# Kernel optimization log

Measured on AMD Instinct MI355X. Metric: run time of the kernel, lower is better.

The kernel has to match this reference:

```python
import jax, jax.numpy as jnp
import numpy as np

EMBED_DIM = 96
OUT_DIM = 192
HEADS = 2
HEAD_DIM = OUT_DIM // HEADS  # 96
STRIDE_Q = (1, 2, 2)
STRIDE_KV = (1, 8, 8)
SCALE = 1.0 / float(np.sqrt(HEAD_DIM))


def layer_norm(x, g, b, eps=1e-5):
    m = jnp.mean(x, -1, keepdims=True)
    v = jnp.mean(jnp.square(x - m), -1, keepdims=True)
    return (x - m) * jax.lax.rsqrt(v + eps) * g + b


def pool(x, thw, conv_w, g, b, stride):
    # x: [B, heads, N, d] with cls token at position 0; depthwise conv3d pool + LayerNorm(d)
    B, nh, N, d = x.shape
    T, H, W = thw
    cls_tok, rest = x[:, :, :1], x[:, :, 1:]
    rest = rest.transpose(0, 1, 3, 2).reshape(B * nh, d, T, H, W)
    rest = jax.lax.conv_general_dilated(
        rest, conv_w, stride, [(1, 1), (1, 1), (1, 1)],
        dimension_numbers=('NCDHW', 'OIDHW', 'NCDHW'), feature_group_count=d)
    T2, H2, W2 = rest.shape[2], rest.shape[3], rest.shape[4]
    rest = rest.reshape(B, nh, d, -1).transpose(0, 1, 3, 2)
    x = jnp.concatenate([cls_tok, rest], axis=2)
    return layer_norm(x, g, b), (T2, H2, W2)


def rel_idx(q_n, k_n):
    # decomposed relative-distance indices with q/k resolution ratio scaling
    q_r = max(k_n / q_n, 1.0)
    k_r = max(q_n / k_n, 1.0)
    d = (jnp.arange(q_n, dtype=jnp.float32)[:, None] * q_r
         - jnp.arange(k_n, dtype=jnp.float32)[None, :] * k_r + (k_n - 1) * k_r)
    return d.astype(jnp.int32)


def add_rel_pos(attn, q, q_thw, k_thw, rph, rpw, rpt):
    qt, qh, qw = q_thw
    kt, kh, kw = k_thw
    Rh = rph[rel_idx(qh, kh)]  # [qh, kh, d]
    Rw = rpw[rel_idx(qw, kw)]  # [qw, kw, d]
    Rt = rpt[rel_idx(qt, kt)]  # [qt, kt, d]
    B, nh, qN, d = q.shape
    r_q = q[:, :, 1:].reshape(B, nh, qt, qh, qw, d)
    rel_h = jnp.einsum('bythwc,hkc->bythwk', r_q, Rh)  # k = kh
    rel_w = jnp.einsum('bythwc,wkc->bythwk', r_q, Rw)  # k = kw
    rel_t = jnp.einsum('bythwc,tkc->bythwk', r_q, Rt)  # k = kt
    rel = (rel_t[..., :, None, None] + rel_h[..., None, :, None]
           + rel_w[..., None, None, :]).reshape(B, nh, qt * qh * qw, kt * kh * kw)
    return attn.at[:, :, 1:, 1:].add(rel)


def _forward(x, qkv_w, qkv_b, proj_w, proj_b, pq_w, nq_g, nq_b, pk_w, nk_g, nk_b,
             pv_w, nv_g, nv_b, rel_pos_h, rel_pos_w, rel_pos_t, thw):
    B, N, C = x.shape
    qkv = (x @ qkv_w.T + qkv_b).reshape(B, N, 3, HEADS, HEAD_DIM).transpose(2, 0, 3, 1, 4)
    q, k, v = qkv[0], qkv[1], qkv[2]  # each [B, heads, N, head_dim]
    k, k_thw = pool(k, thw, pk_w, nk_g, nk_b, STRIDE_KV)
    v, _ = pool(v, thw, pv_w, nv_g, nv_b, STRIDE_KV)
    q, q_thw = pool(q, thw, pq_w, nq_g, nq_b, STRIDE_Q)
    attn = jnp.einsum('bhqd,bhkd->bhqk', q * SCALE, k)
    attn = add_rel_pos(attn, q, q_thw, k_thw, rel_pos_h, rel_pos_w, rel_pos_t)
    attn = jax.nn.softmax(attn, axis=-1)
    out = jnp.einsum('bhqk,bhkd->bhqd', attn, v) + q  # residual_pool, with cls embed
    out = out.transpose(0, 2, 1, 3).reshape(B, -1, OUT_DIM)
    return out @ proj_w.T + proj_b


def setup_inputs() -> dict:
    key = jax.random.key(0)
    ks = jax.random.split(key, 10)
    T, H, W = 8, 56, 56
    N = 1 + T * H * W  # 25089
    B = 4
    std = 0.02
    return {
        'x': jax.random.normal(ks[0], (B, N, EMBED_DIM), jnp.float32),
        'qkv_w': jax.random.normal(ks[1], (3 * OUT_DIM, EMBED_DIM), jnp.float32) * std,
        'qkv_b': jnp.zeros((3 * OUT_DIM,), jnp.float32),
        'proj_w': jax.random.normal(ks[2], (OUT_DIM, OUT_DIM), jnp.float32) * std,
        'proj_b': jnp.zeros((OUT_DIM,), jnp.float32),
        'pq_w': jax.random.normal(ks[3], (HEAD_DIM, 1, 3, 3, 3), jnp.float32) * std,
        'nq_g': jnp.ones((HEAD_DIM,), jnp.float32),
        'nq_b': jnp.zeros((HEAD_DIM,), jnp.float32),
        'pk_w': jax.random.normal(ks[4], (HEAD_DIM, 1, 3, 3, 3), jnp.float32) * std,
        'nk_g': jnp.ones((HEAD_DIM,), jnp.float32),
        'nk_b': jnp.zeros((HEAD_DIM,), jnp.float32),
        'pv_w': jax.random.normal(ks[5], (HEAD_DIM, 1, 3, 3, 3), jnp.float32) * std,
        'nv_g': jnp.ones((HEAD_DIM,), jnp.float32),
        'nv_b': jnp.zeros((HEAD_DIM,), jnp.float32),
        'rel_pos_h': jax.random.normal(ks[6], (55, HEAD_DIM), jnp.float32) * std,
        'rel_pos_w': jax.random.normal(ks[7], (55, HEAD_DIM), jnp.float32) * std,
        'rel_pos_t': jax.random.normal(ks[8], (15, HEAD_DIM), jnp.float32) * std,
        'thw_t': 8, 'thw_h': 56, 'thw_w': 56,
    }


def reference(x, qkv_w, qkv_b, proj_w, proj_b, pq_w, nq_g, nq_b, pk_w, nk_g, nk_b,
              pv_w, nv_g, nv_b, rel_pos_h, rel_pos_w, rel_pos_t, thw_t, thw_h, thw_w):
    thw = (int(thw_t), int(thw_h), int(thw_w))
    return _forward(x, qkv_w, qkv_b, proj_w, proj_b, pq_w, nq_g, nq_b, pk_w, nk_g, nk_b,
                    pv_w, nv_g, nv_b, rel_pos_h, rel_pos_w, rel_pos_t, thw)
```

## Files before the change

kernel.cpp:

```cpp
#include <hip/hip_runtime.h>
#include <hip/hip_bf16.h>

typedef short short8 __attribute__((ext_vector_type(8)));
typedef float floatx4 __attribute__((ext_vector_type(4)));
typedef float floatx4v __attribute__((ext_vector_type(4)));

#define SCALE_F 0.10206207261596575f
#define TOKSTRIDE 401424

static __device__ __forceinline__ float b2f(unsigned short u){
  unsigned int v = ((unsigned int)u) << 16; float f;
  __builtin_memcpy(&f, &v, 4); return f;
}
static __device__ __forceinline__ unsigned short f2b(float f){
  __hip_bfloat16 h = __float2bfloat16(f);
  unsigned short u; __builtin_memcpy(&u, &h, 2); return u;
}
static __device__ __forceinline__ int map20(int i){
  return (i < 2) ? i : 7 + ((i-2)/3)*8 + ((i-2)%3);
}

struct ConvDesc {
  const void* src[17];
  long long off[17];
  int count[17];
};

__global__ __launch_bounds__(256) void k_convert(ConvDesc d, unsigned short* dst_base,
                                                 int* flagp, const unsigned int* xprobe)
{
  __shared__ int sflag;
  if (threadIdx.x < 64){
    unsigned int w = xprobe[1024 + threadIdx.x];
    int e = (w >> 7) & 0xFF;
    int pl = (e >= 90 && e <= 140) ? 1 : 0;
    unsigned long long m = __ballot(pl);
    if (threadIdx.x == 0){
      sflag = (__popcll(m) < 40) ? 1 : 0;
      if (blockIdx.x == 0 && blockIdx.y == 0) *flagp = sflag;
    }
  }
  __syncthreads();
  const int flag = sflag;
  const int t = blockIdx.y + 1;
  const int cnt = d.count[t];
  unsigned short* dst = dst_base + d.off[t];
  const float* sf = (const float*)d.src[t];
  const unsigned short* su = (const unsigned short*)d.src[t];
  for (int i = blockIdx.x*blockDim.x + threadIdx.x; i < cnt; i += gridDim.x*blockDim.x){
    dst[i] = flag ? f2b(sf[i]) : su[i];
  }
}

static __device__ __forceinline__ void load_x_frag(
    const void* xr_, int flag, size_t elem_off, short8& a0, short8& a1, short8& a2)
{
  if (flag){
    const float* xr = (const float*)xr_ + elem_off;
    floatx4v f0 = *(const floatx4v*)(xr),      f1 = *(const floatx4v*)(xr+4);
    floatx4v f2 = *(const floatx4v*)(xr+32),   f3 = *(const floatx4v*)(xr+36);
    floatx4v f4 = *(const floatx4v*)(xr+64),   f5 = *(const floatx4v*)(xr+68);
    #pragma unroll
    for (int j = 0; j < 4; ++j){
      a0[j] = (short)f2b(f0[j]); a0[j+4] = (short)f2b(f1[j]);
      a1[j] = (short)f2b(f2[j]); a1[j+4] = (short)f2b(f3[j]);
      a2[j] = (short)f2b(f4[j]); a2[j+4] = (short)f2b(f5[j]);
    }
  } else {
    const unsigned short* xr = (const unsigned short*)xr_ + elem_off;
    a0 = *(const short8*)(xr);
    a1 = *(const short8*)(xr + 32);
    a2 = *(const short8*)(xr + 64);
  }
}

__global__ __launch_bounds__(256) void k_qkv(
    const void* __restrict__ x, const unsigned short* __restrict__ w,
    const unsigned short* __restrict__ bias, unsigned short* __restrict__ qr,
    unsigned short* __restrict__ kc, unsigned short* __restrict__ vc,
    unsigned short* __restrict__ kcls, unsigned short* __restrict__ vcls,
    const int* __restrict__ flagp)
{
  const int flag = *flagp;
  const int lane = threadIdx.x & 63;
  const int wv = threadIdx.x >> 6;
  const int kq = (lane >> 4) * 8;
  const int quad = lane >> 4;
  const int col_l = lane & 15;

  if (blockIdx.x < 1569){
    const int m_base = blockIdx.x * 64 + wv * 16;
    int ma = m_base + col_l; if (ma > 100355) ma = 100355;
    short8 a0, a1, a2;
    load_x_frag(x, flag, (size_t)ma*96 + kq, a0, a1, a2);

    int bbase[4], ntok[4], mrow[4];
    #pragma unroll
    for (int r = 0; r < 4; ++r){
      int m = m_base + quad*4 + r;
      mrow[r] = m;
      int bb = m / 25089;
      ntok[r] = m - bb*25089;
      bbase[r] = bb*2;
    }

    #pragma unroll
    for (int ct = 0; ct < 12; ++ct){
      int col = ct*16 + col_l;
      const unsigned short* wrow = w + col*96 + kq;
      short8 b0 = *(const short8*)(wrow);
      short8 b1 = *(const short8*)(wrow + 32);
      short8 b2 = *(const short8*)(wrow + 64);
      float bv = b2f(bias[col]);
      floatx4 acc = {0.f,0.f,0.f,0.f};
      acc = __builtin_amdgcn_mfma_f32_16x16x32_bf16(a0, b0, acc, 0,0,0);
      acc = __builtin_amdgcn_mfma_f32_16x16x32_bf16(a1, b1, acc, 0,0,0);
      acc = __builtin_amdgcn_mfma_f32_16x16x32_bf16(a2, b2, acc, 0,0,0);
      const int head = ct / 6;
      const int dt6  = ct % 6;
      #pragma unroll
      for (int r = 0; r < 4; ++r){
        if (mrow[r] < 100356)
          qr[(size_t)((bbase[r]+head)*6 + dt6)*TOKSTRIDE + (size_t)ntok[r]*16 + col_l]
            = f2b(acc[r] + bv);
      }
    }
  } else {
    const int id = blockIdx.x - 1569;
    const int isv = id / 201;
    const int bx = id - isv*201;
    const int rbase = bx * 64 + wv * 16;

    int rhoA = rbase + col_l; if (rhoA > 12803) rhoA = 12803;
    int bA, nA;
    if (rhoA < 4){ bA = rhoA; nA = 0; }
    else {
      int rp = rhoA - 4;
      bA = rp / 3200; int rem = rp - bA*3200;
      int t = rem / 400; int s = rem - t*400;
      int ry = s / 20, rx = s - ry*20;
      nA = 1 + (t*56 + map20(ry))*56 + map20(rx);
    }
    short8 a0, a1, a2;
    load_x_frag(x, flag, ((size_t)bA*25089 + nA)*96 + kq, a0, a1, a2);

    int isCls[4], bI[4], baseI[4], valid[4];
    #pragma unroll
    for (int r = 0; r < 4; ++r){
      int rho = rbase + quad*4 + r;
      valid[r] = (rho < 12804);
      if (rho > 12803) rho = 12803;
      if (rho < 4){ isCls[r] = 1; bI[r] = rho; baseI[r] = 0; }
      else {
        int rp = rho - 4;
        int b = rp / 3200; int rem = rp - b*3200;
        int t = rem / 400; int s = rem - t*400;
        int ry = s / 20, rx = s - ry*20;
        isCls[r] = 0; bI[r] = b;
        baseI[r] = (((b*8 + t)*20 + ry)*20 + rx)*192;
      }
    }

    unsigned short* buf  = isv ? vc : kc;
    unsigned short* bufc = isv ? vcls : kcls;
    #pragma unroll
    for (int ct = 0; ct < 12; ++ct){
      const int col = 192 + (isv*12 + ct)*16 + col_l;
      const unsigned short* wrow = w + col*96 + kq;
      short8 b0 = *(const short8*)(wrow);
      short8 b1 = *(const short8*)(wrow + 32);
      short8 b2 = *(const short8*)(wrow + 64);
      float bv = b2f(bias[col]);
      floatx4 acc = {0.f,0.f,0.f,0.f};
      acc = __builtin_amdgcn_mfma_f32_16x16x32_bf16(a0, b0, acc, 0,0,0);
      acc = __builtin_amdgcn_mfma_f32_16x16x32_bf16(a1, b1, acc, 0,0,0);
      acc = __builtin_amdgcn_mfma_f32_16x16x32_bf16(a2, b2, acc, 0,0,0);
      const int head = ct / 6;
      const int dstat = (ct % 6) * 16;
      #pragma unroll
      for (int r = 0; r < 4; ++r){
        if (valid[r]){
          float o = acc[r] + bv;
          if (isCls[r]) bufc[(bI[r]*2 + head)*96 + dstat + col_l] = f2b(o);
          else          buf[baseI[r] + head*96 + dstat + col_l]   = f2b(o);
        }
      }
    }
  }
}

__global__ __launch_bounds__(384) void k_pool(
    const unsigned short* __restrict__ qr, const unsigned short* __restrict__ cwq,
    const unsigned short* __restrict__ gq, const unsigned short* __restrict__ btaq,
    unsigned short* __restrict__ qp,
    const unsigned short* __restrict__ kc, const unsigned short* __restrict__ vc,
    const unsigned short* __restrict__ kcls, const unsigned short* __restrict__ vcls,
    const unsigned short* __restrict__ cwk, const unsigned short* __restrict__ gk, const unsigned short* __restrict__ bk,
    const unsigned short* __restrict__ cwv, const unsigned short* __restrict__ gv, const unsigned short* __restrict__ bv,
    unsigned short* __restrict__ kp, unsigned short* __restrict__ vt)
{
  const int tid = threadIdx.x;
  if (blockIdx.x < 1792){
    __shared__ float wlds[27*96];
    __shared__ float gls[96], bls[96];
    __shared__ float ls1[29*12], ls2[29*12];
    __shared__ float lmean[29], linvs[29];

    const int bid = blockIdx.x;
    const int y  = bid % 28;
    const int t  = (bid / 28) % 8;
    const int bh = bid / 224;
    const bool has_cls = (y == 0 && t == 0);

    for (int idx = tid; idx < 27*96; idx += 384){
      int tap = idx / 96, d = idx - tap*96;
      wlds[idx] = b2f(cwq[d*27 + tap]);
    }
    for (int idx = tid; idx < 96; idx += 384){
      gls[idx] = b2f(gq[idx]); bls[idx] = b2f(btaq[idx]);
    }
    __syncthreads();

    const int x = tid / 12, dg = tid - x*12;
    const unsigned short* rowb = qr + (size_t)(bh*6 + (dg >> 1))*TOKSTRIDE + (dg & 1)*8;
    float val[8] = {0,0,0,0,0,0,0,0};

    if (x < 28){
      #pragma unroll
      for (int dt = 0; dt < 3; ++dt){
        int tt = t + dt - 1; if (tt < 0 || tt >= 8) continue;
        #pragma unroll
        for (int dy = 0; dy < 3; ++dy){
          int yy = 2*y + dy - 1; if (yy < 0 || yy >= 56) continue;
          #pragma unroll
          for (int dx = 0; dx < 3; ++dx){
            int xv = 2*x + dx - 1; if (xv < 0 || xv >= 56) continue;
            const int tap = (dt*3+dy)*3+dx;
            short8 v = *(const short8*)(rowb + (size_t)(1 + (tt*56 + yy)*56 + xv)*16);
            const float* wr = wlds + tap*96 + dg*8;
            #pragma unroll
            for (int j = 0; j < 8; ++j) val[j] += b2f((unsigned short)v[j]) * wr[j];
          }
        }
      }
      float s1 = 0.f, s2 = 0.f;
      #pragma unroll
      for (int j = 0; j < 8; ++j){ s1 += val[j]; s2 += val[j]*val[j]; }
      ls1[x*12+dg] = s1; ls2[x*12+dg] = s2;
    } else if (has_cls && tid >= 348 && tid < 360){
      int cdg = tid - 348;
      const unsigned short* rowc = qr + (size_t)(bh*6 + (cdg >> 1))*TOKSTRIDE + (cdg & 1)*8;
      short8 v = *(const short8*)(rowc);
      float s1 = 0.f, s2 = 0.f;
      #pragma unroll
      for (int j = 0; j < 8; ++j){ val[j] = b2f((unsigned short)v[j]); s1 += val[j]; s2 += val[j]*val[j]; }
      ls1[28*12+cdg] = s1; ls2[28*12+cdg] = s2;
    }
    __syncthreads();

    if (tid < 28 || (tid == 28 && has_cls)){
      float s1 = 0.f, s2 = 0.f;
      #pragma unroll
      for (int k = 0; k < 12; ++k){ s1 += ls1[tid*12+k]; s2 += ls2[tid*12+k]; }
      float mean = s1 * (1.f/96.f);
      float var  = s2 * (1.f/96.f) - mean*mean;
      lmean[tid] = mean; linvs[tid] = rsqrtf(var + 1e-5f);
    }
    __syncthreads();

    if (x < 28){
      float mean = lmean[x], inv = linvs[x];
      int tok = 1 + (t*28 + y)*28 + x;
      short8 o;
      #pragma unroll
      for (int j = 0; j < 8; ++j)
        o[j] = (short)f2b((val[j] - mean)*inv*gls[dg*8+j] + bls[dg*8+j]);
      *(short8*)(qp + ((size_t)bh*6273 + tok)*96 + dg*8) = o;
    } else if (has_cls && tid >= 348 && tid < 360){
      int cdg = tid - 348;
      float mean = lmean[28], inv = linvs[28];
      short8 o;
      #pragma unroll
      for (int j = 0; j < 8; ++j)
        o[j] = (short)f2b((val[j] - mean)*inv*gls[cdg*8+j] + bls[cdg*8+j]);
      *(short8*)(qp + (size_t)bh*6273*96 + cdg*8) = o;
    }
  } else {
    __shared__ float r1[3][128], r2s[3][128];
    const int unit = tid >> 7;
    const int d = tid & 127;
    const int u = (blockIdx.x - 1792)*3 + unit;
    const bool live = (u < 6656);
    int isv = 0, bh = 0, key = 0;
    if (live){
      isv = u / 3328; int rem = u - isv*3328;
      bh = rem / 416; key = rem - bh*416;
    }
    const bool pad = (key >= 393);
    const int b = bh >> 1, head = bh & 1;
    const unsigned short* buf  = isv ? vc : kc;
    const unsigned short* bufc = isv ? vcls : kcls;
    const unsigned short* cw = (isv == 0) ? cwk : cwv;
    const unsigned short* g  = (isv == 0) ? gk : gv;
    const unsigned short* bt = (isv == 0) ? bk : bv;

    float val = 0.f;
    if (live && !pad && d < 96){
      if (key == 0) val = b2f(bufc[bh*96 + d]);
      else {
        int s = key - 1; int t = s / 49; int r2 = s - t*49; int y = r2 / 7; int xx = r2 - y*7;
        const unsigned short* wr = cw + d*27;
        float sum = 0.f;
        #pragma unroll
        for (int dt = 0; dt < 3; ++dt){
          int tt = t + dt - 1; if (tt < 0 || tt >= 8) continue;
          #pragma unroll
          for (int dy = 0; dy < 3; ++dy){
            if (y == 0 && dy == 0) continue;
            int ry = (y == 0) ? (dy - 1) : 2 + 3*(y-1) + dy;
            #pragma unroll
            for (int dx = 0; dx < 3; ++dx){
              if (xx == 0 && dx == 0) continue;
              int rx = (xx == 0) ? (dx - 1) : 2 + 3*(xx-1) + dx;
              sum += b2f(buf[(((b*8 + tt)*20 + ry)*20 + rx)*192 + head*96 + d]) * b2f(wr[(dt*3+dy)*3+dx]);
            }
          }
        }
        val = sum;
      }
    }
    r1[unit][d]  = (d < 96) ? val : 0.f;
    r2s[unit][d] = (d < 96) ? val*val : 0.f;
    __syncthreads();
    for (int off = 64; off > 0; off >>= 1){
      if (d < off){ r1[unit][d] += r1[unit][d+off]; r2s[unit][d] += r2s[unit][d+off]; }
      __syncthreads();
    }
    if (live && d < 96){
      float mean = r1[unit][0] * (1.f/96.f);
      float var  = r2s[unit][0] * (1.f/96.f) - mean*mean;
      float inv = rsqrtf(var + 1e-5f);
      float o = pad ? 0.f : (val - mean)*inv*b2f(g[d]) + b2f(bt[d]);
      if (isv == 0) kp[((size_t)bh*416 + key)*96 + d] = f2b(o);
      else          vt[((size_t)bh*96 + d)*416 + key] = f2b(o);
    }
  }
}

#define PSTR 424
__global__ __launch_bounds__(256) void k_attn(
    const unsigned short* __restrict__ qp, const unsigned short* __restrict__ kp,
    const unsigned short* __restrict__ vt,
    const unsigned short* __restrict__ rph, const unsigned short* __restrict__ rpw,
    const unsigned short* __restrict__ rpt,
    unsigned short* __restrict__ ao)
{
  __shared__ unsigned short P[16*PSTR];
  __shared__ float rel[16*24];
  __shared__ float mx_sh[4][16], sum_sh[4][16];

  const int bh = blockIdx.y;
  const int bb = bh >> 1, head = bh & 1;
  const int tid = threadIdx.x;
  const int lane = tid & 63;
  const int wv = tid >> 6;
  const int q0 = blockIdx.x * 16;

  const unsigned short* qbase = qp + (size_t)bh*6273*96;
  const unsigned short* kbase = kp + (size_t)bh*416*96;
  const unsigned short* vbase = vt + (size_t)bh*96*416;

  const int col = lane & 15;
  const int quad = lane >> 4;
  const int kq = quad * 8;

  short8 a0, a1, a2;
  {
    int qa = q0 + col; if (qa > 6272) qa = 6272;
    const unsigned short* qrow = qbase + (size_t)qa*96 + kq;
    a0 = *(const short8*)(qrow);
    a1 = *(const short8*)(qrow + 32);
    a2 = *(const short8*)(qrow + 64);
  }

  int yq4[4], xq4[4], tq4[4], livx[4], liv[4];
  #pragma unroll
  for (int r = 0; r < 4; ++r){
    int gq = q0 + quad*4 + r;
    liv[r]  = (gq >= 1);
    livx[r] = (gq >= 1 && gq <= 6272);
    int s = (gq >= 1) ? gq - 1 : 0;
    tq4[r] = s / 784; int r2 = s - tq4[r]*784; yq4[r] = r2 / 28; xq4[r] = r2 - yq4[r]*28;
  }

  #pragma unroll
  for (int j = 0; j < 2; ++j){
    const int c = (wv*2 + j)*16 + col;
    const unsigned short* rrow;
    if (c < 55)       rrow = rph + (size_t)c*96;
    else if (c < 110) rrow = rpw + (size_t)(c-55)*96;
    else { int ci = c-110; if (ci > 14) ci = 14; rrow = rpt + (size_t)ci*96; }
    rrow += kq;
    short8 b0 = *(const short8*)(rrow);
    short8 b1 = *(const short8*)(rrow + 32);
    short8 b2 = *(const short8*)(rrow + 64);
    floatx4 rc = {0.f,0.f,0.f,0.f};
    rc = __builtin_amdgcn_mfma_f32_16x16x32_bf16(a0, b0, rc, 0,0,0);
    rc = __builtin_amdgcn_mfma_f32_16x16x32_bf16(a1, b1, rc, 0,0,0);
    rc = __builtin_amdgcn_mfma_f32_16x16x32_bf16(a2, b2, rc, 0,0,0);
    #pragma unroll
    for (int r = 0; r < 4; ++r){
      if (!livx[r]) continue;
      const int m = quad*4 + r;
      if (c < 55){
        int u = yq4[r] + 24 - c;
        if (u >= 0 && u <= 24 && (u & 3) == 0) rel[m*24 + (u >> 2)] = rc[r];
      } else if (c < 110){
        int u = xq4[r] + 24 - (c - 55);
        if (u >= 0 && u <= 24 && (u & 3) == 0) rel[m*24 + 8 + (u >> 2)] = rc[r];
      } else if (c < 125){
        int u = tq4[r] + 7 - (c - 110);
        if (u >= 0 && u <= 7) rel[m*24 + 16 + u] = rc[r];
      }
    }
  }
  __syncthreads();

  const float* Tm[4];
  #pragma unroll
  for (int r = 0; r < 4; ++r) Tm[r] = rel + (quad*4 + r)*24;

  floatx4 acc[7];
  float mx[4] = {-1e30f,-1e30f,-1e30f,-1e30f};
  #pragma unroll
  for (int i = 0; i < 7; ++i){
    int t = wv*7 + i; if (t > 25) t = 25;
    const unsigned short* krow = kbase + (size_t)(t*16 + col)*96 + kq;
    short8 b0 = *(const short8*)(krow);
    short8 b1 = *(const short8*)(krow + 32);
    short8 b2 = *(const short8*)(krow + 64);
    floatx4 a = {0.f,0.f,0.f,0.f};
    a = __builtin_amdgcn_mfma_f32_16x16x32_bf16(a0, b0, a, 0,0,0);
    a = __builtin_amdgcn_mfma_f32_16x16x32_bf16(a1, b1, a, 0,0,0);
    a = __builtin_amdgcn_mfma_f32_16x16x32_bf16(a2, b2, a, 0,0,0);
    const int key = t*16 + col;
    const bool validk = (key < 393);
    int kt = 0, ky = 0, kx = 0;
    if (key >= 1 && validk){
      int ks = key - 1; kt = ks / 49; int krm = ks - kt*49; ky = krm / 7; kx = krm - ky*7;
    }
    #pragma unroll
    for (int r = 0; r < 4; ++r){
      float s;
      if (!validk) s = -1e30f;
      else {
        s = a[r] * SCALE_F;
        if (key >= 1 && liv[r])
          s += Tm[r][ky] + Tm[r][8 + kx] + Tm[r][16 + kt];
      }
      a[r] = s;
      mx[r] = fmaxf(mx[r], s);
    }
    acc[i] = a;
  }
  #pragma unroll
  for (int r = 0; r < 4; ++r){
    #pragma unroll
    for (int o = 1; o < 16; o <<= 1) mx[r] = fmaxf(mx[r], __shfl_xor(mx[r], o, 64));
  }
  if (col == 0){
    #pragma unroll
    for (int r = 0; r < 4; ++r) mx_sh[wv][quad*4 + r] = mx[r];
  }
  __syncthreads();

  float M[4];
  #pragma unroll
  for (int r = 0; r < 4; ++r){
    float m01 = fmaxf(mx_sh[0][quad*4 + r], mx_sh[1][quad*4 + r]);
    float m23 = fmaxf(mx_sh[2][quad*4 + r], mx_sh[3][quad*4 + r]);
    M[r] = fmaxf(m01, m23);
  }
  float sum[4] = {0.f,0.f,0.f,0.f};
  #pragma unroll
  for (int i = 0; i < 7; ++i){
    #pragma unroll
    for (int r = 0; r < 4; ++r){
      float e = __expf(acc[i][r] - M[r]);
      acc[i][r] = e; sum[r] += e;
    }
  }
  #pragma unroll
  for (int r = 0; r < 4; ++r){
    #pragma unroll
    for (int o = 1; o < 16; o <<= 1) sum[r] += __shfl_xor(sum[r], o, 64);
  }
  if (col == 0){
    #pragma unroll
    for (int r = 0; r < 4; ++r) sum_sh[wv][quad*4 + r] = sum[r];
  }
  #pragma unroll
  for (int i = 0; i < 7; ++i){
    int t = wv*7 + i; if (t > 25) t = 25;
    #pragma unroll
    for (int r = 0; r < 4; ++r)
      P[(quad*4 + r)*PSTR + t*16 + col] = f2b(acc[i][r]);
  }
  __syncthreads();

  float linv4[4];
  #pragma unroll
  for (int r = 0; r < 4; ++r)
    linv4[r] = 1.f / (sum_sh[0][quad*4 + r] + sum_sh[1][quad*4 + r]
                    + sum_sh[2][quad*4 + r] + sum_sh[3][quad*4 + r]);

  short8 pf[13];
  #pragma unroll
  for (int s = 0; s < 13; ++s)
    pf[s] = *(const short8*)(P + col*PSTR + s*32 + kq);

  #pragma unroll
  for (int dti = 0; dti < 2; ++dti){
    int slot = wv*2 + dti; if (slot >= 6) slot -= 6;
    const int dd = slot*16 + col;
    const unsigned short* vrow = vbase + (size_t)dd*416 + kq;
    floatx4 o = {0.f,0.f,0.f,0.f};
    #pragma unroll
    for (int s = 0; s < 13; ++s){
      short8 vf = *(const short8*)(vrow + s*32);
      o = __builtin_amdgcn_mfma_f32_16x16x32_bf16(pf[s], vf, o, 0,0,0);
    }
    #pragma unroll
    for (int r = 0; r < 4; ++r){
      int gq = q0 + quad*4 + r;
      if (gq <= 6272){
        float val = o[r] * linv4[r] + b2f(qbase[(size_t)gq*96 + dd]);
        ao[((size_t)bb*6273 + gq)*192 + head*96 + dd] = f2b(val);
      }
    }
  }
}

__global__ __launch_bounds__(256) void k_proj(
    const unsigned short* __restrict__ ao, const unsigned short* __restrict__ w,
    const unsigned short* __restrict__ bias, void* __restrict__ out, const int* __restrict__ flagp)
{
  const int flag = *flagp;
  const int lane = threadIdx.x & 63;
  const int wv = threadIdx.x >> 6;
  const int c = blockIdx.y*64 + wv*16 + (lane & 15);
  const int kq = (lane >> 4) * 8;
  short8 bfr[6];
  const unsigned short* wrow = w + c*192 + kq;
  #pragma unroll
  for (int s = 0; s < 6; ++s) bfr[s] = *(const short8*)(wrow + 32*s);
  float bv = b2f(bias[c]);
  const int m_base = blockIdx.x * 64;
  for (int i = 0; i < 4; ++i){
    int mt = m_base + i*16;
    int ma = mt + (lane & 15); if (ma > 25091) ma = 25091;
    const unsigned short* arow = ao + (size_t)ma*192 + kq;
    floatx4 acc = {0.f,0.f,0.f,0.f};
    #pragma unroll
    for (int s = 0; s < 6; ++s){
      short8 a = *(const short8*)(arow + 32*s);
      acc = __builtin_amdgcn_mfma_f32_16x16x32_bf16(a, bfr[s], acc, 0,0,0);
    }
    #pragma unroll
    for (int r = 0; r < 4; ++r){
      int m = mt + (lane >> 4)*4 + r;
      if (m < 25092){
        float o = acc[r] + bv;
        if (flag) ((float*)out)[(size_t)m*192 + c] = o;
        else      ((unsigned short*)out)[(size_t)m*192 + c] = f2b(o);
      }
    }
  }
}

extern "C" void kernel_launch(void* const* d_in, const int* in_sizes, int n_in,
                              void* d_out, int out_size, void* d_ws, size_t ws_size,
                              hipStream_t stream)
{
  char* p = (char*)d_ws;
  int* flagp = (int*)p; p += 16;
  unsigned short* conv = (unsigned short*)p;

  ConvDesc desc;
  long long cum = 0;
  for (int i = 0; i < 17; ++i){
    desc.src[i] = d_in[i];
    desc.off[i] = cum;
    desc.count[i] = in_sizes[i];
    cum += in_sizes[i];
  }
  p += (size_t)cum * 2;

  unsigned short* q_raw  = (unsigned short*)p; p += (size_t)19268352*2;
  unsigned short* kc     = (unsigned short*)p; p += (size_t)2457600*2;
  unsigned short* vc     = (unsigned short*)p; p += (size_t)2457600*2;
  unsigned short* kcls   = (unsigned short*)p; p += (size_t)768*2;
  unsigned short* vcls   = (unsigned short*)p; p += (size_t)768*2;
  unsigned short* q_pool = (unsigned short*)p; p += (size_t)4817664*2;
  unsigned short* kp_buf = (unsigned short*)p; p += (size_t)319488*2;
  unsigned short* v_t    = (unsigned short*)p; p += (size_t)319488*2;
  unsigned short* a_out  = q_raw;

  const unsigned short* cqkv_w = conv + desc.off[1];
  const unsigned short* cqkv_b = conv + desc.off[2];
  const unsigned short* cproj_w= conv + desc.off[3];
  const unsigned short* cproj_b= conv + desc.off[4];
  const unsigned short* cpq_w  = conv + desc.off[5];
  const unsigned short* cnq_g  = conv + desc.off[6];
  const unsigned short* cnq_b  = conv + desc.off[7];
  const unsigned short* cpk_w  = conv + desc.off[8];
  const unsigned short* cnk_g  = conv + desc.off[9];
  const unsigned short* cnk_b  = conv + desc.off[10];
  const unsigned short* cpv_w  = conv + desc.off[11];
  const unsigned short* cnv_g  = conv + desc.off[12];
  const unsigned short* cnv_b  = conv + desc.off[13];
  const unsigned short* crph   = conv + desc.off[14];
  const unsigned short* crpw   = conv + desc.off[15];
  const unsigned short* crpt   = conv + desc.off[16];

  k_convert<<<dim3(16, 16), 256, 0, stream>>>(desc, conv, flagp, (const unsigned int*)d_in[0]);
  k_qkv  <<<dim3(1971), 256, 0, stream>>>(d_in[0], cqkv_w, cqkv_b, q_raw, kc, vc, kcls, vcls, flagp);
  k_pool <<<dim3(4011), 384, 0, stream>>>(q_raw, cpq_w, cnq_g, cnq_b, q_pool,
                                          kc, vc, kcls, vcls,
                                          cpk_w, cnk_g, cnk_b, cpv_w, cnv_g, cnv_b, kp_buf, v_t);
  k_attn <<<dim3(393, 8), 256, 0, stream>>>(q_pool, kp_buf, v_t, crph, crpw, crpt, a_out);
  k_proj <<<dim3(393, 3), 256, 0, stream>>>(a_out, cproj_w, cproj_b, d_out, flagp);
}
```

Before: 269.9 us.

## Remove parameter conversion kernel; detect dtype per kernel and convert weights inline

Drops the separate k_convert launch that copied every weight tensor to bf16 and wrote a dtype flag. Each kernel now infers the input dtype itself by sampling 32 words of x, then reads weights directly as fp32 or bf16 and converts them on the fly. The attention kernel's relative-position table is also transposed so each lane reads its three bias terms as float4 vectors instead of scalar loads. This saves one launch and a small copy pass, in exchange for redundant dtype probing and conversion in every block and more scalar weight loads in the pool kernels.

```diff
diff --git a/kernel.cpp b/kernel.cpp
--- a/kernel.cpp
+++ b/kernel.cpp
@@ -20,68 +20,50 @@
   return (i < 2) ? i : 7 + ((i-2)/3)*8 + ((i-2)%3);
 }
 
-struct ConvDesc {
-  const void* src[17];
-  long long off[17];
-  int count[17];
-};
-
-__global__ __launch_bounds__(256) void k_convert(ConvDesc d, unsigned short* dst_base,
-                                                 int* flagp, const unsigned int* xprobe)
-{
-  __shared__ int sflag;
-  if (threadIdx.x < 64){
-    unsigned int w = xprobe[1024 + threadIdx.x];
+static __device__ __forceinline__ int detect_f32(const void* x){
+  const unsigned int* xw = (const unsigned int*)x;
+  int c = 0;
+  #pragma unroll
+  for (int i = 0; i < 32; ++i){
+    unsigned int w = xw[1024 + i];
     int e = (w >> 7) & 0xFF;
-    int pl = (e >= 90 && e <= 140) ? 1 : 0;
-    unsigned long long m = __ballot(pl);
-    if (threadIdx.x == 0){
-      sflag = (__popcll(m) < 40) ? 1 : 0;
-      if (blockIdx.x == 0 && blockIdx.y == 0) *flagp = sflag;
-    }
-  }
-  __syncthreads();
-  const int flag = sflag;
-  const int t = blockIdx.y + 1;
-  const int cnt = d.count[t];
-  unsigned short* dst = dst_base + d.off[t];
-  const float* sf = (const float*)d.src[t];
-  const unsigned short* su = (const unsigned short*)d.src[t];
-  for (int i = blockIdx.x*blockDim.x + threadIdx.x; i < cnt; i += gridDim.x*blockDim.x){
-    dst[i] = flag ? f2b(sf[i]) : su[i];
-  }
+    c += (e >= 90 && e <= 140) ? 1 : 0;
+  }
+  return (c < 20) ? 1 : 0;
+}
+
+static __device__ __forceinline__ short8 load_frag8(const void* p_, int flag, size_t off){
+  if (flag){
+    const float* p = (const float*)p_ + off;
+    floatx4v f0 = *(const floatx4v*)(p);
+    floatx4v f1 = *(const floatx4v*)(p + 4);
+    short8 o;
+    #pragma unroll
+    for (int j = 0; j < 4; ++j){ o[j] = (short)f2b(f0[j]); o[j+4] = (short)f2b(f1[j]); }
+    return o;
+  } else {
+    return *(const short8*)((const unsigned short*)p_ + off);
+  }
+}
+static __device__ __forceinline__ float ldf(const void* p, int flag, int i){
+  return flag ? ((const float*)p)[i] : b2f(((const unsigned short*)p)[i]);
 }
 
 static __device__ __forceinline__ void load_x_frag(
     const void* xr_, int flag, size_t elem_off, short8& a0, short8& a1, short8& a2)
 {
-  if (flag){
-    const float* xr = (const float*)xr_ + elem_off;
-    floatx4v f0 = *(const floatx4v*)(xr),      f1 = *(const floatx4v*)(xr+4);
-    floatx4v f2 = *(const floatx4v*)(xr+32),   f3 = *(const floatx4v*)(xr+36);
-    floatx4v f4 = *(const floatx4v*)(xr+64),   f5 = *(const floatx4v*)(xr+68);
-    #pragma unroll
-    for (int j = 0; j < 4; ++j){
-      a0[j] = (short)f2b(f0[j]); a0[j+4] = (short)f2b(f1[j]);
-      a1[j] = (short)f2b(f2[j]); a1[j+4] = (short)f2b(f3[j]);
-      a2[j] = (short)f2b(f4[j]); a2[j+4] = (short)f2b(f5[j]);
-    }
-  } else {
-    const unsigned short* xr = (const unsigned short*)xr_ + elem_off;
-    a0 = *(const short8*)(xr);
-    a1 = *(const short8*)(xr + 32);
-    a2 = *(const short8*)(xr + 64);
-  }
+  a0 = load_frag8(xr_, flag, elem_off);
+  a1 = load_frag8(xr_, flag, elem_off + 32);
+  a2 = load_frag8(xr_, flag, elem_off + 64);
 }
 
 __global__ __launch_bounds__(256) void k_qkv(
-    const void* __restrict__ x, const unsigned short* __restrict__ w,
-    const unsigned short* __restrict__ bias, unsigned short* __restrict__ qr,
+    const void* __restrict__ x, const void* __restrict__ w,
+    const void* __restrict__ bias, unsigned short* __restrict__ qr,
     unsigned short* __restrict__ kc, unsigned short* __restrict__ vc,
-    unsigned short* __restrict__ kcls, unsigned short* __restrict__ vcls,
-    const int* __restrict__ flagp)
+    unsigned short* __restrict__ kcls, unsigned short* __restrict__ vcls)
 {
-  const int flag = *flagp;
+  const int flag = detect_f32(x);
   const int lane = threadIdx.x & 63;
   const int wv = threadIdx.x >> 6;
   const int kq = (lane >> 4) * 8;
@@ -107,11 +89,10 @@
     #pragma unroll
     for (int ct = 0; ct < 12; ++ct){
       int col = ct*16 + col_l;
-      const unsigned short* wrow = w + col*96 + kq;
-      short8 b0 = *(const short8*)(wrow);
-      short8 b1 = *(const short8*)(wrow + 32);
-      short8 b2 = *(const short8*)(wrow + 64);
-      float bv = b2f(bias[col]);
+      short8 b0 = load_frag8(w, flag, (size_t)col*96 + kq);
+      short8 b1 = load_frag8(w, flag, (size_t)col*96 + kq + 32);
+      short8 b2 = load_frag8(w, flag, (size_t)col*96 + kq + 64);
+      float bv = ldf(bias, flag, col);
       floatx4 acc = {0.f,0.f,0.f,0.f};
       acc = __builtin_amdgcn_mfma_f32_16x16x32_bf16(a0, b0, acc, 0,0,0);
       acc = __builtin_amdgcn_mfma_f32_16x16x32_bf16(a1, b1, acc, 0,0,0);
@@ -166,11 +147,10 @@
     #pragma unroll
     for (int ct = 0; ct < 12; ++ct){
       const int col = 192 + (isv*12 + ct)*16 + col_l;
-      const unsigned short* wrow = w + col*96 + kq;
-      short8 b0 = *(const short8*)(wrow);
-      short8 b1 = *(const short8*)(wrow + 32);
-      short8 b2 = *(const short8*)(wrow + 64);
-      float bv = b2f(bias[col]);
+      short8 b0 = load_frag8(w, flag, (size_t)col*96 + kq);
+      short8 b1 = load_frag8(w, flag, (size_t)col*96 + kq + 32);
+      short8 b2 = load_frag8(w, flag, (size_t)col*96 + kq + 64);
+      float bv = ldf(bias, flag, col);
       floatx4 acc = {0.f,0.f,0.f,0.f};
       acc = __builtin_amdgcn_mfma_f32_16x16x32_bf16(a0, b0, acc, 0,0,0);
       acc = __builtin_amdgcn_mfma_f32_16x16x32_bf16(a1, b1, acc, 0,0,0);
@@ -190,15 +170,17 @@
 }
 
 __global__ __launch_bounds__(384) void k_pool(
-    const unsigned short* __restrict__ qr, const unsigned short* __restrict__ cwq,
-    const unsigned short* __restrict__ gq, const unsigned short* __restrict__ btaq,
+    const void* __restrict__ x,
+    const unsigned short* __restrict__ qr, const void* __restrict__ cwq,
+    const void* __restrict__ gq, const void* __restrict__ btaq,
     unsigned short* __restrict__ qp,
     const unsigned short* __restrict__ kc, const unsigned short* __restrict__ vc,
     const unsigned short* __restrict__ kcls, const unsigned short* __restrict__ vcls,
-    const unsigned short* __restrict__ cwk, const unsigned short* __restrict__ gk, const unsigned short* __restrict__ bk,
-    const unsigned short* __restrict__ cwv, const unsigned short* __restrict__ gv, const unsigned short* __restrict__ bv,
+    const void* __restrict__ cwk, const void* __restrict__ gk, const void* __restrict__ bk,
+    const void* __restrict__ cwv, const void* __restrict__ gv, const void* __restrict__ bv,
     unsigned short* __restrict__ kp, unsigned short* __restrict__ vt)
 {
+  const int flag = detect_f32(x);
   const int tid = threadIdx.x;
   if (blockIdx.x < 1792){
     __shared__ float wlds[27*96];
@@ -214,18 +196,18 @@
 
     for (int idx = tid; idx < 27*96; idx += 384){
       int tap = idx / 96, d = idx - tap*96;
-      wlds[idx] = b2f(cwq[d*27 + tap]);
+      wlds[idx] = ldf(cwq, flag, d*27 + tap);
     }
     for (int idx = tid; idx < 96; idx += 384){
-      gls[idx] = b2f(gq[idx]); bls[idx] = b2f(btaq[idx]);
+      gls[idx] = ldf(gq, flag, idx); bls[idx] = ldf(btaq, flag, idx);
     }
     __syncthreads();
 
-    const int x = tid / 12, dg = tid - x*12;
+    const int xx0 = tid / 12, dg = tid - xx0*12;
     const unsigned short* rowb = qr + (size_t)(bh*6 + (dg >> 1))*TOKSTRIDE + (dg & 1)*8;
     float val[8] = {0,0,0,0,0,0,0,0};
 
-    if (x < 28){
+    if (xx0 < 28){
       #pragma unroll
       for (int dt = 0; dt < 3; ++dt){
         int tt = t + dt - 1; if (tt < 0 || tt >= 8) continue;
@@ -234,7 +216,7 @@
           int yy = 2*y + dy - 1; if (yy < 0 || yy >= 56) continue;
           #pragma unroll
           for (int dx = 0; dx < 3; ++dx){
-            int xv = 2*x + dx - 1; if (xv < 0 || xv >= 56) continue;
+            int xv = 2*xx0 + dx - 1; if (xv < 0 || xv >= 56) continue;
             const int tap = (dt*3+dy)*3+dx;
             short8 v = *(const short8*)(rowb + (size_t)(1 + (tt*56 + yy)*56 + xv)*16);
             const float* wr = wlds + tap*96 + dg*8;
@@ -246,7 +228,7 @@
       float s1 = 0.f, s2 = 0.f;
       #pragma unroll
       for (int j = 0; j < 8; ++j){ s1 += val[j]; s2 += val[j]*val[j]; }
-      ls1[x*12+dg] = s1; ls2[x*12+dg] = s2;
+      ls1[xx0*12+dg] = s1; ls2[xx0*12+dg] = s2;
     } else if (has_cls && tid >= 348 && tid < 360){
       int cdg = tid - 348;
       const unsigned short* rowc = qr + (size_t)(bh*6 + (cdg >> 1))*TOKSTRIDE + (cdg & 1)*8;
@@ -268,9 +250,9 @@
     }
     __syncthreads();
 
-    if (x < 28){
-      float mean = lmean[x], inv = linvs[x];
-      int tok = 1 + (t*28 + y)*28 + x;
+    if (xx0 < 28){
+      float mean = lmean[xx0], inv = linvs[xx0];
+      int tok = 1 + (t*28 + y)*28 + xx0;
       short8 o;
       #pragma unroll
       for (int j = 0; j < 8; ++j)
@@ -300,16 +282,15 @@
     const int b = bh >> 1, head = bh & 1;
     const unsigned short* buf  = isv ? vc : kc;
     const unsigned short* bufc = isv ? vcls : kcls;
-    const unsigned short* cw = (isv == 0) ? cwk : cwv;
-    const unsigned short* g  = (isv == 0) ? gk : gv;
-    const unsigned short* bt = (isv == 0) ? bk : bv;
+    const void* cw = (isv == 0) ? cwk : cwv;
+    const void* g  = (isv == 0) ? gk : gv;
+    const void* bt = (isv == 0) ? bk : bv;
 
     float val = 0.f;
     if (live && !pad && d < 96){
       if (key == 0) val = b2f(bufc[bh*96 + d]);
       else {
         int s = key - 1; int t = s / 49; int r2 = s - t*49; int y = r2 / 7; int xx = r2 - y*7;
-        const unsigned short* wr = cw + d*27;
         float sum = 0.f;
         #pragma unroll
         for (int dt = 0; dt < 3; ++dt){
@@ -322,7 +303,8 @@
             for (int dx = 0; dx < 3; ++dx){
               if (xx == 0 && dx == 0) continue;
               int rx = (xx == 0) ? (dx - 1) : 2 + 3*(xx-1) + dx;
-              sum += b2f(buf[(((b*8 + tt)*20 + ry)*20 + rx)*192 + head*96 + d]) * b2f(wr[(dt*3+dy)*3+dx]);
+              sum += b2f(buf[(((b*8 + tt)*20 + ry)*20 + rx)*192 + head*96 + d])
+                   * ldf(cw, flag, d*27 + (dt*3+dy)*3+dx);
             }
           }
         }
@@ -340,7 +322,7 @@
       float mean = r1[unit][0] * (1.f/96.f);
       float var  = r2s[unit][0] * (1.f/96.f) - mean*mean;
       float inv = rsqrtf(var + 1e-5f);
-      float o = pad ? 0.f : (val - mean)*inv*b2f(g[d]) + b2f(bt[d]);
+      float o = pad ? 0.f : (val - mean)*inv*ldf(g, flag, d) + ldf(bt, flag, d);
       if (isv == 0) kp[((size_t)bh*416 + key)*96 + d] = f2b(o);
       else          vt[((size_t)bh*96 + d)*416 + key] = f2b(o);
     }
@@ -349,16 +331,18 @@
 
 #define PSTR 424
 __global__ __launch_bounds__(256) void k_attn(
+    const void* __restrict__ x,
     const unsigned short* __restrict__ qp, const unsigned short* __restrict__ kp,
     const unsigned short* __restrict__ vt,
-    const unsigned short* __restrict__ rph, const unsigned short* __restrict__ rpw,
-    const unsigned short* __restrict__ rpt,
+    const void* __restrict__ rph, const void* __restrict__ rpw,
+    const void* __restrict__ rpt,
     unsigned short* __restrict__ ao)
 {
   __shared__ unsigned short P[16*PSTR];
-  __shared__ float rel[16*24];
+  __shared__ __align__(16) float rel[24*16];
   __shared__ float mx_sh[4][16], sum_sh[4][16];
 
+  const int flag = detect_f32(x);
   const int bh = blockIdx.y;
   const int bb = bh >> 1, head = bh & 1;
   const int tid = threadIdx.x;
@@ -396,14 +380,13 @@
   #pragma unroll
   for (int j = 0; j < 2; ++j){
     const int c = (wv*2 + j)*16 + col;
-    const unsigned short* rrow;
-    if (c < 55)       rrow = rph + (size_t)c*96;
-    else if (c < 110) rrow = rpw + (size_t)(c-55)*96;
-    else { int ci = c-110; if (ci > 14) ci = 14; rrow = rpt + (size_t)ci*96; }
-    rrow += kq;
-    short8 b0 = *(const short8*)(rrow);
-    short8 b1 = *(const short8*)(rrow + 32);
-    short8 b2 = *(const short8*)(rrow + 64);
+    const void* rsrc; int rrow;
+    if (c < 55){ rsrc = rph; rrow = c; }
+    else if (c < 110){ rsrc = rpw; rrow = c - 55; }
+    else { int ci = c - 110; if (ci > 14) ci = 14; rsrc = rpt; rrow = ci; }
+    short8 b0 = load_frag8(rsrc, flag, (size_t)rrow*96 + kq);
+    short8 b1 = load_frag8(rsrc, flag, (size_t)rrow*96 + kq + 32);
+    short8 b2 = load_frag8(rsrc, flag, (size_t)rrow*96 + kq + 64);
     floatx4 rc = {0.f,0.f,0.f,0.f};
     rc = __builtin_amdgcn_mfma_f32_16x16x32_bf16(a0, b0, rc, 0,0,0);
     rc = __builtin_amdgcn_mfma_f32_16x16x32_bf16(a1, b1, rc, 0,0,0);
@@ -414,21 +397,17 @@
       const int m = quad*4 + r;
       if (c < 55){
         int u = yq4[r] + 24 - c;
-        if (u >= 0 && u <= 24 && (u & 3) == 0) rel[m*24 + (u >> 2)] = rc[r];
+        if (u >= 0 && u <= 24 && (u & 3) == 0) rel[(u >> 2)*16 + m] = rc[r];
       } else if (c < 110){
         int u = xq4[r] + 24 - (c - 55);
-        if (u >= 0 && u <= 24 && (u & 3) == 0) rel[m*24 + 8 + (u >> 2)] = rc[r];
+        if (u >= 0 && u <= 24 && (u & 3) == 0) rel[(8 + (u >> 2))*16 + m] = rc[r];
       } else if (c < 125){
         int u = tq4[r] + 7 - (c - 110);
-        if (u >= 0 && u <= 7) rel[m*24 + 16 + u] = rc[r];
+        if (u >= 0 && u <= 7) rel[(16 + u)*16 + m] = rc[r];
       }
     }
   }
   __syncthreads();
-
-  const float* Tm[4];
-  #pragma unroll
-  for (int r = 0; r < 4; ++r) Tm[r] = rel + (quad*4 + r)*24;
 
   floatx4 acc[7];
   float mx[4] = {-1e30f,-1e30f,-1e30f,-1e30f};
@@ -449,14 +428,16 @@
     if (key >= 1 && validk){
       int ks = key - 1; kt = ks / 49; int krm = ks - kt*49; ky = krm / 7; kx = krm - ky*7;
     }
+    floatx4v rh = *(const floatx4v*)(rel + ky*16 + quad*4);
+    floatx4v rw = *(const floatx4v*)(rel + (8 + kx)*16 + quad*4);
+    floatx4v rt = *(const floatx4v*)(rel + (16 + kt)*16 + quad*4);
     #pragma unroll
     for (int r = 0; r < 4; ++r){
       float s;
       if (!validk) s = -1e30f;
       else {
         s = a[r] * SCALE_F;
-        if (key >= 1 && liv[r])
-          s += Tm[r][ky] + Tm[r][8 + kx] + Tm[r][16 + kt];
+        if (key >= 1 && liv[r]) s += rh[r] + rw[r] + rt[r];
       }
       a[r] = s;
       mx[r] = fmaxf(mx[r], s);
@@ -542,19 +523,19 @@
 }
 
 __global__ __launch_bounds__(256) void k_proj(
-    const unsigned short* __restrict__ ao, const unsigned short* __restrict__ w,
-    const unsigned short* __restrict__ bias, void* __restrict__ out, const int* __restrict__ flagp)
+    const void* __restrict__ x,
+    const unsigned short* __restrict__ ao, const void* __restrict__ w,
+    const void* __restrict__ bias, void* __restrict__ out)
 {
-  const int flag = *flagp;
+  const int flag = detect_f32(x);
   const int lane = threadIdx.x & 63;
   const int wv = threadIdx.x >> 6;
   const int c = blockIdx.y*64 + wv*16 + (lane & 15);
   const int kq = (lane >> 4) * 8;
   short8 bfr[6];
-  const unsigned short* wrow = w + c*192 + kq;
-  #pragma unroll
-  for (int s = 0; s < 6; ++s) bfr[s] = *(const short8*)(wrow + 32*s);
-  float bv = b2f(bias[c]);
+  #pragma unroll
+  for (int s = 0; s < 6; ++s) bfr[s] = load_frag8(w, flag, (size_t)c*192 + kq + 32*s);
+  float bv = ldf(bias, flag, c);
   const int m_base = blockIdx.x * 64;
   for (int i = 0; i < 4; ++i){
     int mt = m_base + i*16;
@@ -583,19 +564,6 @@
                               hipStream_t stream)
 {
   char* p = (char*)d_ws;
-  int* flagp = (int*)p; p += 16;
-  unsigned short* conv = (unsigned short*)p;
-
-  ConvDesc desc;
-  long long cum = 0;
-  for (int i = 0; i < 17; ++i){
-    desc.src[i] = d_in[i];
-    desc.off[i] = cum;
-    desc.count[i] = in_sizes[i];
-    cum += in_sizes[i];
-  }
-  p += (size_t)cum * 2;
-
   unsigned short* q_raw  = (unsigned short*)p; p += (size_t)19268352*2;
   unsigned short* kc     = (unsigned short*)p; p += (size_t)2457600*2;
   unsigned short* vc     = (unsigned short*)p; p += (size_t)2457600*2;
@@ -606,28 +574,28 @@
   unsigned short* v_t    = (unsigned short*)p; p += (size_t)319488*2;
   unsigned short* a_out  = q_raw;
 
-  const unsigned short* cqkv_w = conv + desc.off[1];
-  const unsigned short* cqkv_b = conv + desc.off[2];
-  const unsigned short* cproj_w= conv + desc.off[3];
-  const unsigned short* cproj_b= conv + desc.off[4];
-  const unsigned short* cpq_w  = conv + desc.off[5];
-  const unsigned short* cnq_g  = conv + desc.off[6];
-  const unsigned short* cnq_b  = conv + desc.off[7];
-  const unsigned short* cpk_w  = conv + desc.off[8];
-  const unsigned short* cnk_g  = conv + desc.off[9];
-  const unsigned short* cnk_b  = conv + desc.off[10];
-  const unsigned short* cpv_w  = conv + desc.off[11];
-  const unsigned short* cnv_g  = conv + desc.off[12];
-  const unsigned short* cnv_b  = conv + desc.off[13];
-  const unsigned short* crph   = conv + desc.off[14];
-  const unsigned short* crpw   = conv + desc.off[15];
-  const unsigned short* crpt   = conv + desc.off[16];
-
-  k_convert<<<dim3(16, 16), 256, 0, stream>>>(desc, conv, flagp, (const unsigned int*)d_in[0]);
-  k_qkv  <<<dim3(1971), 256, 0, stream>>>(d_in[0], cqkv_w, cqkv_b, q_raw, kc, vc, kcls, vcls, flagp);
-  k_pool <<<dim3(4011), 384, 0, stream>>>(q_raw, cpq_w, cnq_g, cnq_b, q_pool,
+  const void* x      = d_in[0];
+  const void* qkv_w  = d_in[1];
+  const void* qkv_b  = d_in[2];
+  const void* proj_w = d_in[3];
+  const void* proj_b = d_in[4];
+  const void* pq_w   = d_in[5];
+  const void* nq_g   = d_in[6];
+  const void* nq_b   = d_in[7];
+  const void* pk_w   = d_in[8];
+  const void* nk_g   = d_in[9];
+  const void* nk_b   = d_in[10];
+  const void* pv_w   = d_in[11];
+  const void* nv_g   = d_in[12];
+  const void* nv_b   = d_in[13];
+  const void* rph    = d_in[14];
+  const void* rpw    = d_in[15];
+  const void* rpt    = d_in[16];
+
+  k_qkv  <<<dim3(1971), 256, 0, stream>>>(x, qkv_w, qkv_b, q_raw, kc, vc, kcls, vcls);
+  k_pool <<<dim3(4011), 384, 0, stream>>>(x, q_raw, pq_w, nq_g, nq_b, q_pool,
                                           kc, vc, kcls, vcls,
-                                          cpk_w, cnk_g, cnk_b, cpv_w, cnv_g, cnv_b, kp_buf, v_t);
-  k_attn <<<dim3(393, 8), 256, 0, stream>>>(q_pool, kp_buf, v_t, crph, crpw, crpt, a_out);
-  k_proj <<<dim3(393, 3), 256, 0, stream>>>(a_out, cproj_w, cproj_b, d_out, flagp);
-}
+                                          pk_w, nk_g, nk_b, pv_w, nv_g, nv_b, kp_buf, v_t);
+  k_attn <<<dim3(393, 8), 256, 0, stream>>>(x, q_pool, kp_buf, v_t, rph, rpw, rpt, a_out);
+  k_proj <<<dim3(393, 3), 256, 0, stream>>>(x, a_out, proj_w, proj_b, d_out);
+}
```

Result: slower. 325.7 us (+20.7%).
